# Kernel tuning notes

Measured on AMD Instinct MI355X. Metric: run time of the kernel, lower is better.

Reference implementation:

```python
import jax, jax.numpy as jnp
import numpy as np

H_DIM = 1024
N_HEADS = 16
SEQ_LEN = 2048
BATCH = 4


def setup_inputs() -> dict:
    key = jax.random.key(0)
    ks = jax.random.split(key, 9)
    s = 1.0 / np.sqrt(H_DIM)
    return {
        "x": jax.random.normal(ks[0], (BATCH, SEQ_LEN, H_DIM), dtype=jnp.float32),
        "Wq": jax.random.normal(ks[1], (H_DIM, H_DIM), dtype=jnp.float32) * s,
        "bq": jax.random.normal(ks[2], (H_DIM,), dtype=jnp.float32) * 0.01,
        "Wk": jax.random.normal(ks[3], (H_DIM, H_DIM), dtype=jnp.float32) * s,
        "bk": jax.random.normal(ks[4], (H_DIM,), dtype=jnp.float32) * 0.01,
        "Wv": jax.random.normal(ks[5], (H_DIM, H_DIM), dtype=jnp.float32) * s,
        "bv": jax.random.normal(ks[6], (H_DIM,), dtype=jnp.float32) * 0.01,
        "Wo": jax.random.normal(ks[7], (H_DIM, H_DIM), dtype=jnp.float32) * s,
        "bo": jax.random.normal(ks[8], (H_DIM,), dtype=jnp.float32) * 0.01,
    }


def reference(x, Wq, bq, Wk, bk, Wv, bv, Wo, bo):
    B, T, C = x.shape
    N = N_HEADS
    D = C // N
    # projections -> [B, N, T, D]
    def split_heads(t):
        return t.reshape(B, T, N, D).transpose(0, 2, 1, 3)
    q = split_heads(x @ Wq + bq)
    k = split_heads(x @ Wk + bk)
    v = split_heads(x @ Wv + bv)
    scale = 1.0 / jnp.sqrt(jnp.asarray(D, dtype=x.dtype))
    logits = jnp.einsum("bntd,bnsd->bnts", q, k) * scale  # [B,N,T,T]
    causal = jnp.tril(jnp.ones((T, T), dtype=bool))
    logits = jnp.where(causal[None, None], logits, jnp.asarray(-jnp.inf, dtype=x.dtype))
    attn = jax.nn.softmax(logits, axis=-1)
    ctx = jnp.einsum("bnts,bnsd->bntd", attn, v)  # [B,N,T,D]
    ctx = ctx.transpose(0, 2, 1, 3).reshape(B, T, C)
    return ctx @ Wo + bo
```

## Files before the change

kernel.cpp:

```cpp
#include <hip/hip_runtime.h>
#include <hip/hip_bf16.h>


typedef __attribute__((ext_vector_type(8))) short bhalf8;
typedef __attribute__((ext_vector_type(4))) float f32x4;

#define BATCH 4
#define SEQ 2048
#define CDIM 1024
#define NHEAD 16
#define HDIM 64
#define MTOT (BATCH * SEQ)
#define QSCALE 0.18033688011112042f

static __device__ inline unsigned short f2bf(float f) {
    unsigned int u = __float_as_uint(f);
    unsigned int r = (u + 0x7fffu + ((u >> 16) & 1u)) >> 16;
    return (unsigned short)r;
}
static __device__ inline float bf2f(unsigned short u) {
    return __uint_as_float(((unsigned int)u) << 16);
}
static __device__ inline f32x4 zero4() {
    f32x4 z = {0.f, 0.f, 0.f, 0.f};
    return z;
}
static __device__ inline f32x4 MFMA(bhalf8 a, bhalf8 b, f32x4 c) {
    return __builtin_amdgcn_mfma_f32_16x16x32_bf16(a, b, c, 0, 0, 0);
}
static __device__ inline void gload16(const void* g, void* l) {
    __builtin_amdgcn_global_load_lds(
        (const __attribute__((address_space(1))) unsigned int*)g,
        (__attribute__((address_space(3))) unsigned int*)l, 16, 0, 0);
}
static __device__ inline unsigned int pkbf16(float lo, float hi) {
    union { __hip_bfloat162 h; unsigned int u; } c;
    c.h = __float22bfloat162_rn(make_float2(lo, hi));
    return c.u;
}

__global__ __launch_bounds__(256) void cast_x_kernel(const float* __restrict__ x,
                                                     short* __restrict__ o, int n8) {
    int i = blockIdx.x * 256 + threadIdx.x;
    if (i >= n8) return;
    const float4* xv = (const float4*)x;
    float4 a = xv[i * 2];
    float4 b = xv[i * 2 + 1];
    bhalf8 r;
    r[0] = (short)f2bf(a.x); r[1] = (short)f2bf(a.y);
    r[2] = (short)f2bf(a.z); r[3] = (short)f2bf(a.w);
    r[4] = (short)f2bf(b.x); r[5] = (short)f2bf(b.y);
    r[6] = (short)f2bf(b.z); r[7] = (short)f2bf(b.w);
    *(bhalf8*)(o + (size_t)i * 8) = r;
}

__global__ __launch_bounds__(256) void wtrans_kernel(const float* __restrict__ W0,
                                                     const float* __restrict__ W1,
                                                     const float* __restrict__ W2,
                                                     const float* __restrict__ W3,
                                                     short* __restrict__ out) {
    __shared__ float t[32][33];
    const float* W = (blockIdx.z == 0) ? W0 : (blockIdx.z == 1) ? W1
                     : (blockIdx.z == 2) ? W2 : W3;
    short* o = out + (size_t)blockIdx.z * CDIM * CDIM;
    int n0 = blockIdx.x * 32, k0 = blockIdx.y * 32;
    int tx = threadIdx.x, ty = threadIdx.y;
    for (int j = 0; j < 4; ++j)
        t[ty + j * 8][tx] = W[(size_t)(k0 + ty + j * 8) * CDIM + n0 + tx];
    __syncthreads();
    for (int j = 0; j < 4; ++j)
        o[(size_t)(n0 + ty + j * 8) * CDIM + k0 + tx] = (short)f2bf(t[tx][ty + j * 8]);
}

template <int MODE, int GN>
__global__ __launch_bounds__(512) void gemm256(const short* __restrict__ A,
                                               const short* __restrict__ Bt,
                                               const float* __restrict__ b0,
                                               const float* __restrict__ b1,
                                               const float* __restrict__ b2,
                                               unsigned short* __restrict__ QKout,
                                               unsigned short* __restrict__ Vout,
                                               float* __restrict__ Fout) {
    __shared__ char lds[65536];
    char* AlB0 = lds;
    char* BlB0 = lds + 32768;

    const int tid = threadIdx.x, lane = tid & 63, w = tid >> 6;
    const int g = lane >> 4, t16 = lane & 15;
    const int wr = w >> 2, wc = w & 3;

    const int f = blockIdx.x;
    const int xcd = f & 7, i = f >> 3;
    const int mt = xcd * 4 + i / GN, nt = i % GN;
    const int tm = mt * 256, tn = nt * 256;
    const int part = nt >> 2;

    const int c0 = tid, c1 = 512 + tid;
    const int r0 = c0 >> 2, r1 = c1 >> 2;
    const int k0c = (c0 & 3) ^ ((r0 >> 1) & 3);
    const int k1c = (c1 & 3) ^ ((r1 >> 1) & 3);
    const short* a0 = A + (size_t)(tm + r0) * 1024 + k0c * 8;
    const short* a1 = A + (size_t)(tm + r1) * 1024 + k1c * 8;
    const short* bp0 = Bt + (size_t)(tn + r0) * 1024 + k0c * 8;
    const short* bp1 = Bt + (size_t)(tn + r1) * 1024 + k1c * 8;

    int aoff[8], boff[4];
#pragma unroll
    for (int mi = 0; mi < 8; ++mi) {
        int row = wr * 128 + mi * 16 + t16;
        aoff[mi] = row * 64 + ((g ^ ((row >> 1) & 3)) << 4);
    }
#pragma unroll
    for (int ni = 0; ni < 4; ++ni) {
        int row = wc * 64 + ni * 16 + t16;
        boff[ni] = row * 64 + ((g ^ ((row >> 1) & 3)) << 4);
    }

    f32x4 acc[8][4];
#pragma unroll
    for (int mi = 0; mi < 8; ++mi)
#pragma unroll
        for (int ni = 0; ni < 4; ++ni) acc[mi][ni] = zero4();

#define STAGE(kt_, bb_)                                                   \
    do {                                                                  \
        int off_ = (kt_) * 32;                                            \
        char* al_ = AlB0 + (bb_) * 16384;                                 \
        char* bl_ = BlB0 + (bb_) * 16384;                                 \
        gload16(a0 + off_, al_ + w * 1024);                               \
        gload16(a1 + off_, al_ + 8192 + w * 1024);                        \
        gload16(bp0 + off_, bl_ + w * 1024);                              \
        gload16(bp1 + off_, bl_ + 8192 + w * 1024);                       \
    } while (0)

    STAGE(0, 0);
    __syncthreads();

#pragma unroll 2
    for (int kt = 0; kt < 32; ++kt) {
        const int buf = kt & 1;
        if (kt + 1 < 32) STAGE(kt + 1, buf ^ 1);
        const char* al = AlB0 + buf * 16384;
        const char* bl = BlB0 + buf * 16384;
        bhalf8 af[8], bfr[4];
#pragma unroll
        for (int mi = 0; mi < 8; ++mi) af[mi] = *(const bhalf8*)(al + aoff[mi]);
#pragma unroll
        for (int ni = 0; ni < 4; ++ni) bfr[ni] = *(const bhalf8*)(bl + boff[ni]);
        __builtin_amdgcn_s_setprio(1);
#pragma unroll
        for (int mi = 0; mi < 8; ++mi)
#pragma unroll
            for (int ni = 0; ni < 4; ++ni)
                acc[mi][ni] = MFMA(af[mi], bfr[ni], acc[mi][ni]);
        __builtin_amdgcn_s_setprio(0);
        __syncthreads();
    }
#undef STAGE

    for (int h = 0; h < 2; ++h) {
        if (h) __syncthreads();
        if (MODE == 0 && part == 2) {
            if (wr == h) {
#pragma unroll
                for (int mi = 0; mi < 8; ++mi)
#pragma unroll
                    for (int ni = 0; ni < 4; ++ni) {
                        int col = wc * 64 + ni * 16 + t16;
                        float bias = b2[(tn + col) & 1023];
#pragma unroll
                        for (int r = 0; r < 4; ++r) {
                            int m_l = mi * 16 + g * 4 + r;
                            int byte = col * 256 + ((m_l * 2) ^ ((col & 7) << 4));
                            *(unsigned short*)(lds + byte) = f2bf(acc[mi][ni][r] + bias);
                        }
                    }
            }
            __syncthreads();
#pragma unroll
            for (int p = 0; p < 8; ++p) {
                int lin = p * 8192 + tid * 16;
                int rv = lin >> 8;
                int inrow = lin & 255;
                int phys = rv * 256 + (inrow ^ ((rv & 7) << 4));
                bhalf8 val = *(const bhalf8*)(lds + phys);
                int m0 = inrow >> 1;
                int n_g = tn + rv;
                int hh = (n_g & 1023) >> 6, d = n_g & 63;
                int m = tm + h * 128 + m0;
                int bi = m >> 11, t0 = m & 2047;
                *(bhalf8*)(Vout + (((size_t)((bi * NHEAD + hh) * HDIM + d)) << 11) + t0) = val;
            }
        } else {
            if (wr == h) {
#pragma unroll
                for (int mi = 0; mi < 8; ++mi)
#pragma unroll
                    for (int ni = 0; ni < 4; ++ni) {
                        int col = wc * 64 + ni * 16 + t16;
                        float bias = 0.f;
                        if (MODE == 0) bias = (part == 0 ? b0 : b1)[(tn + col) & 1023];
#pragma unroll
                        for (int r = 0; r < 4; ++r) {
                            int row_l = mi * 16 + g * 4 + r;
                            float v = acc[mi][ni][r] + bias;
                            if (MODE == 0 && part == 0) v *= QSCALE;
                            int byte = row_l * 512 + ((col * 2) ^ (((row_l >> 2) & 3) << 5));
                            *(unsigned short*)(lds + byte) = f2bf(v);
                        }
                    }
            }
            __syncthreads();
#pragma unroll
            for (int p = 0; p < 8; ++p) {
                int lin = p * 8192 + tid * 16;
                int row_l = lin >> 9;
                int inrow = lin & 511;
                int phys = row_l * 512 + ((inrow & ~31) ^ (((row_l >> 2) & 3) << 5)) + (inrow & 31);
                bhalf8 val = *(const bhalf8*)(lds + phys);
                int col0 = inrow >> 1;
                int n_g = tn + col0;
                int m = tm + h * 128 + row_l;
                if (MODE == 1) {
                    float* op = Fout + (size_t)m * 1024 + n_g;
                    float4 o0, o1;
                    o0.x = bf2f((unsigned short)val[0]) + b0[n_g + 0];
                    o0.y = bf2f((unsigned short)val[1]) + b0[n_g + 1];
                    o0.z = bf2f((unsigned short)val[2]) + b0[n_g + 2];
                    o0.w = bf2f((unsigned short)val[3]) + b0[n_g + 3];
                    o1.x = bf2f((unsigned short)val[4]) + b0[n_g + 4];
                    o1.y = bf2f((unsigned short)val[5]) + b0[n_g + 5];
                    o1.z = bf2f((unsigned short)val[6]) + b0[n_g + 6];
                    o1.w = bf2f((unsigned short)val[7]) + b0[n_g + 7];
                    *(float4*)(op) = o0;
                    *(float4*)(op + 4) = o1;
                } else {
                    int bi = m >> 11, t = m & 2047;
                    int hh = (n_g & 1023) >> 6, d0 = n_g & 63;
                    *(bhalf8*)(QKout +
                               (((size_t)((part * 64 + bi * NHEAD + hh) * SEQ + t)) << 6) + d0) = val;
                }
            }
        }
    }
}

__global__ __launch_bounds__(256) void attn_kernel(const short* __restrict__ Q,
                                                   const short* __restrict__ K,
                                                   const short* __restrict__ V,
                                                   unsigned short* __restrict__ ctx) {
    __shared__ short Kl[2][64 * 64];
    __shared__ short Vl[2][64 * 64];
    __shared__ short Pl[4][32 * 64];

    const int tid = threadIdx.x, lane = tid & 63, w = tid >> 6;
    const int g = lane >> 4, t16 = lane & 15;

    int orig = blockIdx.x;
    int swz = (orig & 7) * 64 + (orig >> 3);
    const int bh = swz >> 3;
    const int sp = swz & 7;

    const short* Qh = Q + ((size_t)bh << 17);
    const short* Kh = K + ((size_t)bh << 17);
    const short* Vh = V + ((size_t)bh << 17);

    int koff[2], voff[2], ldst[2];
#pragma unroll
    for (int it = 0; it < 2; ++it) {
        int c = it * 256 + tid;
        int srow = c >> 3;
        int dc = (c & 7) ^ (srow & 7);
        koff[it] = (srow << 6) + dc * 8;
        voff[it] = (srow << 11) + dc * 8;
        ldst[it] = it * 4096 + w * 1024;
    }

#define STAGE(kv_, bb_)                                                       \
    do {                                                                      \
        gload16(Kh + koff[0] + ((kv_) << 12), (char*)Kl[bb_] + ldst[0]);      \
        gload16(Kh + koff[1] + ((kv_) << 12), (char*)Kl[bb_] + ldst[1]);      \
        gload16(Vh + voff[0] + ((kv_) << 6), (char*)Vl[bb_] + ldst[0]);       \
        gload16(Vh + voff[1] + ((kv_) << 6), (char*)Vl[bb_] + ldst[1]);       \
    } while (0)

    const int b = bh >> 4, hh = bh & 15;

    STAGE(0, 0);

    for (int ph = 0; ph < 2; ++ph) {
        const int qti = (ph == 0) ? (15 - sp) : sp;
        const int qbase = qti * 128;
        const int ntile = 2 * qti + 2;

        bhalf8 qf[2][2];
#pragma unroll
        for (int nf = 0; nf < 2; ++nf) {
            const short* qp = Qh + ((size_t)(qbase + w * 32 + nf * 16 + t16) << 6) + g * 8;
            qf[nf][0] = *(const bhalf8*)(qp);
            qf[nf][1] = *(const bhalf8*)(qp + 32);
        }

        f32x4 acc[2][4];
#pragma unroll
        for (int rf = 0; rf < 2; ++rf)
#pragma unroll
            for (int i = 0; i < 4; ++i) acc[rf][i] = zero4();
        float m[2], l[2];
        m[0] = m[1] = -1e30f;
        l[0] = l[1] = 0.f;

        __syncthreads();

        int buf = 0;
        for (int kv = 0; kv < ntile; ++kv) {
            if (kv + 1 < ntile) STAGE(kv + 1, buf ^ 1);

            f32x4 lg[2][4];
            __builtin_amdgcn_s_setprio(1);
#pragma unroll
            for (int cb = 0; cb < 4; ++cb) {
                int s = cb * 16 + t16;
                int sw = (s & 7) << 4;
                const char* rowp = (const char*)Kl[buf] + s * 128;
                bhalf8 k0 = *(const bhalf8*)(rowp + ((g * 16) ^ sw));
                bhalf8 k1 = *(const bhalf8*)(rowp + ((64 + g * 16) ^ sw));
#pragma unroll
                for (int nf = 0; nf < 2; ++nf) {
                    f32x4 z = zero4();
                    z = MFMA(k0, qf[nf][0], z);
                    z = MFMA(k1, qf[nf][1], z);
                    lg[nf][cb] = z;
                }
            }
            __builtin_amdgcn_s_setprio(0);

            if (kv >= 2 * qti) {
#pragma unroll
                for (int nf = 0; nf < 2; ++nf) {
                    int row = qbase + w * 32 + nf * 16 + t16;
#pragma unroll
                    for (int cb = 0; cb < 4; ++cb) {
                        int key0 = kv * 64 + cb * 16 + g * 4;
#pragma unroll
                        for (int r = 0; r < 4; ++r)
                            if (key0 + r > row) lg[nf][cb][r] = -1e30f;
                    }
                }
            }

            float pm[2];
#pragma unroll
            for (int nf = 0; nf < 2; ++nf) {
                float a = fmaxf(fmaxf(lg[nf][0][0], lg[nf][0][1]),
                                fmaxf(lg[nf][0][2], lg[nf][0][3]));
                float bb = fmaxf(fmaxf(lg[nf][1][0], lg[nf][1][1]),
                                 fmaxf(lg[nf][1][2], lg[nf][1][3]));
                float c = fmaxf(fmaxf(lg[nf][2][0], lg[nf][2][1]),
                                fmaxf(lg[nf][2][2], lg[nf][2][3]));
                float d = fmaxf(fmaxf(lg[nf][3][0], lg[nf][3][1]),
                                fmaxf(lg[nf][3][2], lg[nf][3][3]));
                float t = fmaxf(fmaxf(a, bb), fmaxf(c, d));
                t = fmaxf(t, __shfl_xor(t, 16, 64));
                t = fmaxf(t, __shfl_xor(t, 32, 64));
                pm[nf] = t;
            }

            bool need = (pm[0] > m[0] + 8.f) || (pm[1] > m[1] + 8.f);
            if (__any(need)) {
                float corr[2];
#pragma unroll
                for (int nf = 0; nf < 2; ++nf) {
                    float mn = fmaxf(m[nf], pm[nf]);
                    corr[nf] = exp2f(m[nf] - mn);
                    m[nf] = mn;
                    l[nf] *= corr[nf];
                }
#pragma unroll
                for (int rf = 0; rf < 2; ++rf)
#pragma unroll
                    for (int r = 0; r < 4; ++r) {
                        float c = __shfl(corr[rf], g * 4 + r, 64);
#pragma unroll
                        for (int db = 0; db < 4; ++db) acc[rf][db][r] *= c;
                    }
            }

#pragma unroll
            for (int nf = 0; nf < 2; ++nf) {
                float s_ = 0.f;
                int rowbyte = (nf * 16 + t16) * 128;
                int swb = (t16 & 7) << 4;
#pragma unroll
                for (int cb = 0; cb < 4; ++cb) {
                    float e0 = exp2f(lg[nf][cb][0] - m[nf]);
                    float e1 = exp2f(lg[nf][cb][1] - m[nf]);
                    float e2 = exp2f(lg[nf][cb][2] - m[nf]);
                    float e3 = exp2f(lg[nf][cb][3] - m[nf]);
                    s_ += (e0 + e1) + (e2 + e3);
                    uint2 wv;
                    wv.x = pkbf16(e0, e1);
                    wv.y = pkbf16(e2, e3);
                    int byte = (rowbyte + cb * 32 + g * 8) ^ swb;
                    *(uint2*)((char*)Pl[w] + byte) = wv;
                }
                l[nf] += s_;
            }

            __builtin_amdgcn_s_setprio(1);
#pragma unroll
            for (int kk = 0; kk < 2; ++kk) {
                bhalf8 vf[4];
#pragma unroll
                for (int db = 0; db < 4; ++db) {
                    int d = db * 16 + t16;
                    int vbyte = d * 128 + ((kk * 64 + g * 16) ^ ((d & 7) << 4));
                    vf[db] = *(const bhalf8*)((const char*)Vl[buf] + vbyte);
                }
#pragma unroll
                for (int rf = 0; rf < 2; ++rf) {
                    int lr2 = rf * 16 + t16;
                    int abyte = (lr2 * 128 + kk * 64 + g * 16) ^ ((lr2 & 7) << 4);
                    bhalf8 pa = *(const bhalf8*)((const char*)Pl[w] + abyte);
#pragma unroll
                    for (int db = 0; db < 4; ++db)
                        acc[rf][db] = MFMA(pa, vf[db], acc[rf][db]);
                }
            }
            __builtin_amdgcn_s_setprio(0);

            __syncthreads();
            buf ^= 1;
        }

        if (ph == 0) STAGE(0, 0);

        float linv[2];
#pragma unroll
        for (int nf = 0; nf < 2; ++nf) {
            float t = l[nf];
            t += __shfl_xor(t, 16, 64);
            t += __shfl_xor(t, 32, 64);
            linv[nf] = 1.f / t;
        }
#pragma unroll
        for (int rf = 0; rf < 2; ++rf)
#pragma unroll
            for (int r = 0; r < 4; ++r) {
                float inv = __shfl(linv[rf], g * 4 + r, 64);
                int t = qbase + w * 32 + rf * 16 + g * 4 + r;
                size_t rowoff = (((size_t)(b * SEQ + t)) << 10) + hh * 64;
#pragma unroll
                for (int db = 0; db < 4; ++db)
                    ctx[rowoff + db * 16 + t16] = f2bf(acc[rf][db][r] * inv);
            }
    }
#undef STAGE
}

extern "C" void kernel_launch(void* const* d_in, const int* in_sizes, int n_in,
                              void* d_out, int out_size, void* d_ws, size_t ws_size,
                              hipStream_t stream) {
    const float* x  = (const float*)d_in[0];
    const float* Wq = (const float*)d_in[1];
    const float* bq = (const float*)d_in[2];
    const float* Wk = (const float*)d_in[3];
    const float* bk = (const float*)d_in[4];
    const float* Wv = (const float*)d_in[5];
    const float* bv = (const float*)d_in[6];
    const float* Wo = (const float*)d_in[7];
    const float* bo = (const float*)d_in[8];

    char* ws = (char*)d_ws;
    short* x16 = (short*)(ws);
    short* Wt  = (short*)(ws + (size_t)16 * 1024 * 1024);
    short* Wot = Wt + (size_t)3 * CDIM * CDIM;
    short* Qb  = (short*)(ws + (size_t)24 * 1024 * 1024);
    short* Vb  = (short*)(ws + (size_t)56 * 1024 * 1024);
    short* Ctx = (short*)(ws + (size_t)72 * 1024 * 1024);

    cast_x_kernel<<<dim3(MTOT * CDIM / 8 / 256), dim3(256), 0, stream>>>(
        x, x16, MTOT * CDIM / 8);
    wtrans_kernel<<<dim3(32, 32, 4), dim3(32, 8), 0, stream>>>(Wq, Wk, Wv, Wo, Wt);

    gemm256<0, 12><<<dim3(384), dim3(512), 0, stream>>>(
        x16, Wt, bq, bk, bv, (unsigned short*)Qb, (unsigned short*)Vb, nullptr);

    attn_kernel<<<dim3(512), dim3(256), 0, stream>>>(
        Qb, Qb + (size_t)64 * SEQ * HDIM, Vb, (unsigned short*)Ctx);

    gemm256<1, 4><<<dim3(128), dim3(512), 0, stream>>>(
        Ctx, Wot, bo, nullptr, nullptr, nullptr, nullptr, (float*)d_out);
}
```

Before: 213.6 us.

## Halve attention query tile to 64 rows and double grid to 1024 blocks

The attention kernel now gives each block 64 query rows instead of 128, so each wave handles 16 rows instead of 32. The grid doubles to 1024 blocks, and the tile pairing becomes (31-sp, sp) over 32 tiles to keep causal work balanced. The causal mask now applies only on the diagonal tile. The prefetch for the second phase now stages into the current buffer instead of buffer 0. The aim is more parallelism, lower register pressure and finer causal skipping. The cost is that each K/V tile loaded into LDS is reused by half as many query rows, which doubles K/V traffic.

```diff
diff --git a/kernel.cpp b/kernel.cpp
--- a/kernel.cpp
+++ b/kernel.cpp
@@ -251,15 +251,15 @@
                                                    unsigned short* __restrict__ ctx) {
     __shared__ short Kl[2][64 * 64];
     __shared__ short Vl[2][64 * 64];
-    __shared__ short Pl[4][32 * 64];
+    __shared__ short Pl[4][16 * 64];
 
     const int tid = threadIdx.x, lane = tid & 63, w = tid >> 6;
     const int g = lane >> 4, t16 = lane & 15;
 
     int orig = blockIdx.x;
-    int swz = (orig & 7) * 64 + (orig >> 3);
-    const int bh = swz >> 3;
-    const int sp = swz & 7;
+    int swz = (orig & 7) * 128 + (orig >> 3);
+    const int bh = swz >> 4;
+    const int sp = swz & 15;
 
     const short* Qh = Q + ((size_t)bh << 17);
     const short* Kh = K + ((size_t)bh << 17);
@@ -285,38 +285,34 @@
     } while (0)
 
     const int b = bh >> 4, hh = bh & 15;
-
+    const int swb = (t16 & 7) << 4;
+
+    int buf = 0;
     STAGE(0, 0);
 
     for (int ph = 0; ph < 2; ++ph) {
-        const int qti = (ph == 0) ? (15 - sp) : sp;
-        const int qbase = qti * 128;
-        const int ntile = 2 * qti + 2;
-
-        bhalf8 qf[2][2];
-#pragma unroll
-        for (int nf = 0; nf < 2; ++nf) {
-            const short* qp = Qh + ((size_t)(qbase + w * 32 + nf * 16 + t16) << 6) + g * 8;
-            qf[nf][0] = *(const bhalf8*)(qp);
-            qf[nf][1] = *(const bhalf8*)(qp + 32);
+        const int qti = (ph == 0) ? (31 - sp) : sp;
+        const int qbase = qti * 64;
+        const int ntile = qti + 1;
+
+        bhalf8 qf0, qf1;
+        {
+            const short* qp = Qh + ((size_t)(qbase + w * 16 + t16) << 6) + g * 8;
+            qf0 = *(const bhalf8*)(qp);
+            qf1 = *(const bhalf8*)(qp + 32);
         }
 
-        f32x4 acc[2][4];
-#pragma unroll
-        for (int rf = 0; rf < 2; ++rf)
-#pragma unroll
-            for (int i = 0; i < 4; ++i) acc[rf][i] = zero4();
-        float m[2], l[2];
-        m[0] = m[1] = -1e30f;
-        l[0] = l[1] = 0.f;
+        f32x4 acc[4];
+#pragma unroll
+        for (int i = 0; i < 4; ++i) acc[i] = zero4();
+        float m = -1e30f, l = 0.f;
 
         __syncthreads();
 
-        int buf = 0;
         for (int kv = 0; kv < ntile; ++kv) {
             if (kv + 1 < ntile) STAGE(kv + 1, buf ^ 1);
 
-            f32x4 lg[2][4];
+            f32x4 lg[4];
             __builtin_amdgcn_s_setprio(1);
 #pragma unroll
             for (int cb = 0; cb < 4; ++cb) {
@@ -325,78 +321,54 @@
                 const char* rowp = (const char*)Kl[buf] + s * 128;
                 bhalf8 k0 = *(const bhalf8*)(rowp + ((g * 16) ^ sw));
                 bhalf8 k1 = *(const bhalf8*)(rowp + ((64 + g * 16) ^ sw));
-#pragma unroll
-                for (int nf = 0; nf < 2; ++nf) {
-                    f32x4 z = zero4();
-                    z = MFMA(k0, qf[nf][0], z);
-                    z = MFMA(k1, qf[nf][1], z);
-                    lg[nf][cb] = z;
+                f32x4 z = zero4();
+                z = MFMA(k0, qf0, z);
+                z = MFMA(k1, qf1, z);
+                lg[cb] = z;
+            }
+            __builtin_amdgcn_s_setprio(0);
+
+            if (kv == qti) {
+                int rowl = w * 16 + t16;
+#pragma unroll
+                for (int cb = 0; cb < 4; ++cb) {
+                    int key0 = cb * 16 + g * 4;
+#pragma unroll
+                    for (int r = 0; r < 4; ++r)
+                        if (key0 + r > rowl) lg[cb][r] = -1e30f;
                 }
             }
-            __builtin_amdgcn_s_setprio(0);
-
-            if (kv >= 2 * qti) {
-#pragma unroll
-                for (int nf = 0; nf < 2; ++nf) {
-                    int row = qbase + w * 32 + nf * 16 + t16;
-#pragma unroll
-                    for (int cb = 0; cb < 4; ++cb) {
-                        int key0 = kv * 64 + cb * 16 + g * 4;
-#pragma unroll
-                        for (int r = 0; r < 4; ++r)
-                            if (key0 + r > row) lg[nf][cb][r] = -1e30f;
-                    }
+
+            float a0 = fmaxf(fmaxf(lg[0][0], lg[0][1]), fmaxf(lg[0][2], lg[0][3]));
+            float a1 = fmaxf(fmaxf(lg[1][0], lg[1][1]), fmaxf(lg[1][2], lg[1][3]));
+            float a2 = fmaxf(fmaxf(lg[2][0], lg[2][1]), fmaxf(lg[2][2], lg[2][3]));
+            float a3 = fmaxf(fmaxf(lg[3][0], lg[3][1]), fmaxf(lg[3][2], lg[3][3]));
+            float pm = fmaxf(fmaxf(a0, a1), fmaxf(a2, a3));
+            pm = fmaxf(pm, __shfl_xor(pm, 16, 64));
+            pm = fmaxf(pm, __shfl_xor(pm, 32, 64));
+
+            if (__any(pm > m + 8.f)) {
+                float mn = fmaxf(m, pm);
+                float corr = exp2f(m - mn);
+                m = mn;
+                l *= corr;
+#pragma unroll
+                for (int r = 0; r < 4; ++r) {
+                    float c = __shfl(corr, g * 4 + r, 64);
+#pragma unroll
+                    for (int db = 0; db < 4; ++db) acc[db][r] *= c;
                 }
             }
 
-            float pm[2];
-#pragma unroll
-            for (int nf = 0; nf < 2; ++nf) {
-                float a = fmaxf(fmaxf(lg[nf][0][0], lg[nf][0][1]),
-                                fmaxf(lg[nf][0][2], lg[nf][0][3]));
-                float bb = fmaxf(fmaxf(lg[nf][1][0], lg[nf][1][1]),
-                                 fmaxf(lg[nf][1][2], lg[nf][1][3]));
-                float c = fmaxf(fmaxf(lg[nf][2][0], lg[nf][2][1]),
-                                fmaxf(lg[nf][2][2], lg[nf][2][3]));
-                float d = fmaxf(fmaxf(lg[nf][3][0], lg[nf][3][1]),
-                                fmaxf(lg[nf][3][2], lg[nf][3][3]));
-                float t = fmaxf(fmaxf(a, bb), fmaxf(c, d));
-                t = fmaxf(t, __shfl_xor(t, 16, 64));
-                t = fmaxf(t, __shfl_xor(t, 32, 64));
-                pm[nf] = t;
-            }
-
-            bool need = (pm[0] > m[0] + 8.f) || (pm[1] > m[1] + 8.f);
-            if (__any(need)) {
-                float corr[2];
-#pragma unroll
-                for (int nf = 0; nf < 2; ++nf) {
-                    float mn = fmaxf(m[nf], pm[nf]);
-                    corr[nf] = exp2f(m[nf] - mn);
-                    m[nf] = mn;
-                    l[nf] *= corr[nf];
-                }
-#pragma unroll
-                for (int rf = 0; rf < 2; ++rf)
-#pragma unroll
-                    for (int r = 0; r < 4; ++r) {
-                        float c = __shfl(corr[rf], g * 4 + r, 64);
-#pragma unroll
-                        for (int db = 0; db < 4; ++db) acc[rf][db][r] *= c;
-                    }
-            }
-
-#pragma unroll
-            for (int nf = 0; nf < 2; ++nf) {
+            {
                 float s_ = 0.f;
-                int rowbyte = (nf * 16 + t16) * 128;
-                int swb = (t16 & 7) << 4;
+                int rowbyte = t16 * 128;
 #pragma unroll
                 for (int cb = 0; cb < 4; ++cb) {
-                    float e0 = exp2f(lg[nf][cb][0] - m[nf]);
-                    float e1 = exp2f(lg[nf][cb][1] - m[nf]);
-                    float e2 = exp2f(lg[nf][cb][2] - m[nf]);
-                    float e3 = exp2f(lg[nf][cb][3] - m[nf]);
+                    float e0 = exp2f(lg[cb][0] - m);
+                    float e1 = exp2f(lg[cb][1] - m);
+                    float e2 = exp2f(lg[cb][2] - m);
+                    float e3 = exp2f(lg[cb][3] - m);
                     s_ += (e0 + e1) + (e2 + e3);
                     uint2 wv;
                     wv.x = pkbf16(e0, e1);
@@ -404,7 +376,7 @@
                     int byte = (rowbyte + cb * 32 + g * 8) ^ swb;
                     *(uint2*)((char*)Pl[w] + byte) = wv;
                 }
-                l[nf] += s_;
+                l += s_;
             }
 
             __builtin_amdgcn_s_setprio(1);
@@ -417,15 +389,11 @@
                     int vbyte = d * 128 + ((kk * 64 + g * 16) ^ ((d & 7) << 4));
                     vf[db] = *(const bhalf8*)((const char*)Vl[buf] + vbyte);
                 }
-#pragma unroll
-                for (int rf = 0; rf < 2; ++rf) {
-                    int lr2 = rf * 16 + t16;
-                    int abyte = (lr2 * 128 + kk * 64 + g * 16) ^ ((lr2 & 7) << 4);
-                    bhalf8 pa = *(const bhalf8*)((const char*)Pl[w] + abyte);
-#pragma unroll
-                    for (int db = 0; db < 4; ++db)
-                        acc[rf][db] = MFMA(pa, vf[db], acc[rf][db]);
-                }
+                int abyte = (t16 * 128 + kk * 64 + g * 16) ^ swb;
+                bhalf8 pa = *(const bhalf8*)((const char*)Pl[w] + abyte);
+#pragma unroll
+                for (int db = 0; db < 4; ++db)
+                    acc[db] = MFMA(pa, vf[db], acc[db]);
             }
             __builtin_amdgcn_s_setprio(0);
 
@@ -433,27 +401,21 @@
             buf ^= 1;
         }
 
-        if (ph == 0) STAGE(0, 0);
-
-        float linv[2];
-#pragma unroll
-        for (int nf = 0; nf < 2; ++nf) {
-            float t = l[nf];
-            t += __shfl_xor(t, 16, 64);
-            t += __shfl_xor(t, 32, 64);
-            linv[nf] = 1.f / t;
+        if (ph == 0) STAGE(0, buf);
+
+        float lt = l;
+        lt += __shfl_xor(lt, 16, 64);
+        lt += __shfl_xor(lt, 32, 64);
+        float linv = 1.f / lt;
+#pragma unroll
+        for (int r = 0; r < 4; ++r) {
+            float inv = __shfl(linv, g * 4 + r, 64);
+            int t = qbase + w * 16 + g * 4 + r;
+            size_t rowoff = (((size_t)(b * SEQ + t)) << 10) + hh * 64;
+#pragma unroll
+            for (int db = 0; db < 4; ++db)
+                ctx[rowoff + db * 16 + t16] = f2bf(acc[db][r] * inv);
         }
-#pragma unroll
-        for (int rf = 0; rf < 2; ++rf)
-#pragma unroll
-            for (int r = 0; r < 4; ++r) {
-                float inv = __shfl(linv[rf], g * 4 + r, 64);
-                int t = qbase + w * 32 + rf * 16 + g * 4 + r;
-                size_t rowoff = (((size_t)(b * SEQ + t)) << 10) + hh * 64;
-#pragma unroll
-                for (int db = 0; db < 4; ++db)
-                    ctx[rowoff + db * 16 + t16] = f2bf(acc[rf][db][r] * inv);
-            }
     }
 #undef STAGE
 }
@@ -486,7 +448,7 @@
     gemm256<0, 12><<<dim3(384), dim3(512), 0, stream>>>(
         x16, Wt, bq, bk, bv, (unsigned short*)Qb, (unsigned short*)Vb, nullptr);
 
-    attn_kernel<<<dim3(512), dim3(256), 0, stream>>>(
+    attn_kernel<<<dim3(1024), dim3(256), 0, stream>>>(
         Qb, Qb + (size_t)64 * SEQ * HDIM, Vb, (unsigned short*)Ctx);
 
     gemm256<1, 4><<<dim3(128), dim3(512), 0, stream>>>(
```

Result: no change. 216.1 us (+1.2%).
